# Kernel tuning notes

Hardware: AMD Instinct MI355X
Metric: run time of the kernel (lower is better)

Reference implementation:

```python
import jax, jax.numpy as jnp
import numpy as np

N_NODES = 80000
N_EDGES = 1280000
IN_DIM = 32
EDGE_DIM = 16
HID = 64
DEPTH = 4
BN_EPS = 1e-5
LN_EPS = 1e-5


def setup_inputs() -> dict:
    key = jax.random.key(0)
    ks = jax.random.split(key, 20)
    s = lambda fan: 1.0 / np.sqrt(fan)
    inp = {
        "x": jax.random.normal(ks[0], (N_NODES, IN_DIM), jnp.float32),
        "edge_index": jax.random.randint(ks[1], (2, N_EDGES), 0, N_NODES, jnp.int32),
        "edge_attr": jax.random.normal(ks[2], (N_EDGES, EDGE_DIM), jnp.float32),
        # input embeddings
        "Wx": jax.random.normal(ks[3], (IN_DIM, HID), jnp.float32) * s(IN_DIM),
        "bx": jnp.zeros((HID,), jnp.float32),
        "We": jax.random.normal(ks[4], (EDGE_DIM, HID), jnp.float32) * s(EDGE_DIM),
        "be": jnp.zeros((HID,), jnp.float32),
        # per-layer GIN MLP params (stacked over DEPTH)
        "W1": jax.random.normal(ks[5], (DEPTH, HID, 2 * HID), jnp.float32) * s(HID),
        "b1": jnp.zeros((DEPTH, 2 * HID), jnp.float32),
        "g1": jnp.ones((DEPTH, 2 * HID), jnp.float32),   # BatchNorm gamma
        "bt1": jnp.zeros((DEPTH, 2 * HID), jnp.float32),  # BatchNorm beta
        "W2": jax.random.normal(ks[6], (DEPTH, 2 * HID, HID), jnp.float32) * s(2 * HID),
        "b2": jnp.zeros((DEPTH, HID), jnp.float32),
        "eps": jnp.zeros((DEPTH,), jnp.float32),           # GIN epsilon, init 0
        # per-layer LayerNorm params
        "ln_g": jnp.ones((DEPTH, HID), jnp.float32),
        "ln_b": jnp.zeros((DEPTH, HID), jnp.float32),
    }
    return inp


def reference(x, edge_index, edge_attr, Wx, bx, We, be, W1, b1, g1, bt1, W2, b2, eps, ln_g, ln_b):
    n = x.shape[0]
    h = jax.nn.relu(x @ Wx + bx)                      # [N, HID]
    ea = jax.nn.relu(edge_attr @ We + be)             # [E, HID]
    row, col = edge_index[0], edge_index[1]           # source, target
    L = W1.shape[0]
    for l in range(L):
        # message: relu(x_j + edge_attr), scatter-add into target nodes
        msg = jax.nn.relu(h[row] + ea)                # [E, HID]
        agg = jax.ops.segment_sum(msg, col, num_segments=n)  # [N, HID]
        z = (1.0 + eps[l]) * h + agg
        # GIN MLP: Linear -> BatchNorm(train stats) -> ReLU -> Linear
        z = z @ W1[l] + b1[l]                         # [N, 2*HID]
        mu = z.mean(axis=0)
        var = z.var(axis=0)                           # biased, as torch BN training
        z = (z - mu) * jax.lax.rsqrt(var + BN_EPS) * g1[l] + bt1[l]
        z = jax.nn.relu(z)
        z = z @ W2[l] + b2[l]                         # [N, HID]
        # LayerNorm
        lm = z.mean(axis=-1, keepdims=True)
        lv = z.var(axis=-1, keepdims=True)
        z = (z - lm) * jax.lax.rsqrt(lv + LN_EPS) * ln_g[l] + ln_b[l]
        if l < L - 1:
            z = jax.nn.relu(z)
        h = z
    return h  # JK == 'last'
```

## Files before the change

kernel.cpp:

```cpp
#include <hip/hip_runtime.h>
#include <cstdint>

typedef _Float16 half8 __attribute__((ext_vector_type(8)));
typedef float f32x4 __attribute__((ext_vector_type(4)));

#define NNODES 80000
#define NEDGES 1280000
#define INDIM 32
#define EDIM 16
#define HID 64
#define HID2 128
#define DEPTH 4
#define BN_EPS 1e-5f
#define LN_EPS 1e-5f
#define NB 313

union U16x8 { uint4 v; _Float16 h[8]; };

__global__ __launch_bounds__(256) void k_node_embed(
    const float* __restrict__ x, const float* __restrict__ Wx,
    const float* __restrict__ bx, _Float16* __restrict__ h16) {
    int gw = (blockIdx.x * 256 + threadIdx.x) >> 6;
    int lane = threadIdx.x & 63;
    if (gw >= NNODES) return;
    float xv = (lane < INDIM) ? x[(size_t)gw * INDIM + lane] : 0.f;
    float acc = bx[lane];
#pragma unroll
    for (int k = 0; k < INDIM; k++)
        acc = fmaf(__shfl(xv, k, 64), Wx[k * HID + lane], acc);
    h16[(size_t)gw * HID + lane] = (_Float16)fmaxf(acc, 0.f);
}

__global__ __launch_bounds__(256) void k_prep(
    const float* __restrict__ W1, const float* __restrict__ W2,
    _Float16* __restrict__ w1T, _Float16* __restrict__ w2T) {
    int id = blockIdx.x * 256 + threadIdx.x;
    if (id < DEPTH * 128 * 64) {
        int l = id / 8192, r = id % 8192, n = r / 64, k = r % 64;
        w1T[id] = (_Float16)W1[(size_t)l * 8192 + k * 128 + n];
    } else {
        int idx = id - DEPTH * 128 * 64;
        int l = idx / 8192, r = idx % 8192, n = r / 128, k = r % 128;
        w2T[idx] = (_Float16)W2[(size_t)l * 8192 + k * 64 + n];
    }
}

__global__ __launch_bounds__(256) void k_hist(const int* __restrict__ col, int* __restrict__ deg) {
    int e = blockIdx.x * 256 + threadIdx.x;
    if (e < NEDGES) atomicAdd(&deg[col[e]], 1);
}

__global__ __launch_bounds__(256) void k_scan1(const int* __restrict__ deg, int* __restrict__ bsum) {
    __shared__ int s[256];
    int i = blockIdx.x * 256 + threadIdx.x;
    int v = (i < NNODES) ? deg[i] : 0;
    s[threadIdx.x] = v;
    __syncthreads();
    for (int o = 128; o > 0; o >>= 1) {
        if (threadIdx.x < o) s[threadIdx.x] += s[threadIdx.x + o];
        __syncthreads();
    }
    if (threadIdx.x == 0) bsum[blockIdx.x] = s[0];
}

__global__ __launch_bounds__(512) void k_scan2(const int* __restrict__ bsum, int* __restrict__ boff) {
    __shared__ int s[512];
    int t = threadIdx.x;
    s[t] = (t < NB) ? bsum[t] : 0;
    __syncthreads();
    for (int o = 1; o < 512; o <<= 1) {
        int v = (t >= o) ? s[t - o] : 0;
        __syncthreads();
        s[t] += v;
        __syncthreads();
    }
    if (t < NB) boff[t] = (t == 0) ? 0 : s[t - 1];
}

__global__ __launch_bounds__(256) void k_scan3(const int* __restrict__ deg,
                                               const int* __restrict__ boff,
                                               int* __restrict__ row_off) {
    __shared__ int s[256];
    int i = blockIdx.x * 256 + threadIdx.x;
    int t = threadIdx.x;
    int v = (i < NNODES) ? deg[i] : 0;
    s[t] = v;
    __syncthreads();
    for (int o = 1; o < 256; o <<= 1) {
        int u = (t >= o) ? s[t - o] : 0;
        __syncthreads();
        s[t] += u;
        __syncthreads();
    }
    int incl = s[t];
    if (i < NNODES) row_off[i] = boff[blockIdx.x] + incl - v;
    if (i == NNODES - 1) row_off[NNODES] = boff[blockIdx.x] + incl;
}

__global__ __launch_bounds__(256) void k_copy(const int* __restrict__ src, int* __restrict__ dst) {
    int i = blockIdx.x * 256 + threadIdx.x;
    if (i < NNODES) dst[i] = src[i];
}

__global__ __launch_bounds__(256) void k_scatter(const int* __restrict__ row,
                                                 const int* __restrict__ col,
                                                 int* __restrict__ cursor,
                                                 int* __restrict__ srow,
                                                 int* __restrict__ seid) {
    int e = blockIdx.x * 256 + threadIdx.x;
    if (e < NEDGES) {
        int c = col[e];
        int pos = atomicAdd(&cursor[c], 1);
        srow[pos] = row[e];
        seid[pos] = e;
    }
}

__global__ __launch_bounds__(256) void k_edge_embed(
    const float* __restrict__ eat, const int* __restrict__ seid,
    const float* __restrict__ We, const float* __restrict__ be,
    _Float16* __restrict__ eas) {
    __shared__ float wT[HID * EDIM];
    __shared__ float bs[HID];
    for (int i = threadIdx.x; i < HID * EDIM; i += 256) {
        int k = i & 15, o = i >> 4;
        wT[i] = We[k * HID + o];
    }
    if (threadIdx.x < HID) bs[threadIdx.x] = be[threadIdx.x];
    __syncthreads();
    int e = blockIdx.x * 256 + threadIdx.x;
    if (e >= NEDGES) return;
    int src = seid[e];
    const float4* ar = (const float4*)(eat + (size_t)src * EDIM);
    float4 a0 = ar[0], a1 = ar[1], a2 = ar[2], a3 = ar[3];
    float ev[16] = {a0.x, a0.y, a0.z, a0.w, a1.x, a1.y, a1.z, a1.w,
                    a2.x, a2.y, a2.z, a2.w, a3.x, a3.y, a3.z, a3.w};
    uint32_t outp[32];
#pragma unroll
    for (int o2 = 0; o2 < 32; o2++) {
        float acc[2];
#pragma unroll
        for (int half = 0; half < 2; half++) {
            int o = o2 * 2 + half;
            const float4* w4 = (const float4*)&wT[o * 16];
            float4 w0 = w4[0], w1 = w4[1], w2 = w4[2], w3 = w4[3];
            float p0 = fmaf(ev[3], w0.w, fmaf(ev[2], w0.z, fmaf(ev[1], w0.y, ev[0] * w0.x)));
            float p1 = fmaf(ev[7], w1.w, fmaf(ev[6], w1.z, fmaf(ev[5], w1.y, ev[4] * w1.x)));
            float p2 = fmaf(ev[11], w2.w, fmaf(ev[10], w2.z, fmaf(ev[9], w2.y, ev[8] * w2.x)));
            float p3 = fmaf(ev[15], w3.w, fmaf(ev[14], w3.z, fmaf(ev[13], w3.y, ev[12] * w3.x)));
            acc[half] = fmaxf(bs[o] + ((p0 + p1) + (p2 + p3)), 0.f);
        }
        union { _Float16 h[2]; uint32_t u; } pk;
        pk.h[0] = (_Float16)acc[0];
        pk.h[1] = (_Float16)acc[1];
        outp[o2] = pk.u;
    }
    uint4* dst = (uint4*)(eas + (size_t)e * HID);
#pragma unroll
    for (int q = 0; q < 8; q++)
        dst[q] = make_uint4(outp[q * 4], outp[q * 4 + 1], outp[q * 4 + 2], outp[q * 4 + 3]);
}

__global__ __launch_bounds__(256) void k_msg(
    const _Float16* __restrict__ h16, const int* __restrict__ row_off,
    const int* __restrict__ srow, const _Float16* __restrict__ eas,
    const float* __restrict__ epsp, _Float16* __restrict__ zc16) {
    int gw = (blockIdx.x * 256 + threadIdx.x) >> 6;
    int lane = threadIdx.x & 63;
    if (gw >= NNODES) return;
    int beg = row_off[gw], end = row_off[gw + 1];
    float acc = 0.f;
    int e = beg;
    for (; e + 7 < end; e += 8) {
        int j[8];
#pragma unroll
        for (int u = 0; u < 8; u++) j[u] = srow[e + u];
        float hv[8], ev[8];
#pragma unroll
        for (int u = 0; u < 8; u++) hv[u] = (float)h16[(size_t)j[u] * HID + lane];
#pragma unroll
        for (int u = 0; u < 8; u++) ev[u] = (float)eas[(size_t)(e + u) * HID + lane];
        float t0 = fmaxf(hv[0] + ev[0], 0.f) + fmaxf(hv[1] + ev[1], 0.f);
        float t1 = fmaxf(hv[2] + ev[2], 0.f) + fmaxf(hv[3] + ev[3], 0.f);
        float t2 = fmaxf(hv[4] + ev[4], 0.f) + fmaxf(hv[5] + ev[5], 0.f);
        float t3 = fmaxf(hv[6] + ev[6], 0.f) + fmaxf(hv[7] + ev[7], 0.f);
        acc += (t0 + t1) + (t2 + t3);
    }
    for (; e < end; ++e) {
        int j = srow[e];
        float hv = (float)h16[(size_t)j * HID + lane];
        float ev = (float)eas[(size_t)e * HID + lane];
        acc += fmaxf(hv + ev, 0.f);
    }
    float epsl = *epsp;
    float hv0 = (float)h16[(size_t)gw * HID + lane];
    zc16[(size_t)gw * HID + lane] = (_Float16)((1.f + epsl) * hv0 + acc);
}

__global__ __launch_bounds__(256) void k_gemm1(
    const _Float16* __restrict__ zc16, const _Float16* __restrict__ w1Tl,
    const float* __restrict__ b1l, _Float16* __restrict__ z1,
    float* __restrict__ bn_acc) {
    __shared__ __align__(16) unsigned char At[64 * 128];
    __shared__ __align__(16) unsigned char Bt[128 * 128];
    __shared__ float red[4][HID2][2];
    int tid = threadIdx.x;
    int nb = blockIdx.x * 64;
#pragma unroll
    for (int i = 0; i < 2; i++) {
        int id = tid + 256 * i;
        int node = id >> 3, c = id & 7;
        uint4 v = *(const uint4*)(zc16 + (size_t)(nb + node) * HID + c * 8);
        *(uint4*)(At + node * 128 + ((c ^ (node & 7)) << 4)) = v;
    }
#pragma unroll
    for (int i = 0; i < 4; i++) {
        int id = tid + 256 * i;
        int r = id >> 3, c = id & 7;
        uint4 v = *(const uint4*)(w1Tl + (size_t)r * HID + c * 8);
        *(uint4*)(Bt + r * 128 + ((c ^ (r & 7)) << 4)) = v;
    }
    __syncthreads();
    int lane = tid & 63, w = tid >> 6;
    int rl = lane & 15, b = lane >> 4;
    f32x4 acc[8];
#pragma unroll
    for (int t = 0; t < 8; t++) acc[t] = (f32x4){0.f, 0.f, 0.f, 0.f};
#pragma unroll
    for (int s = 0; s < 2; s++) {
        int arow = w * 16 + rl;
        half8 af = *(const half8*)(At + arow * 128 + (((s * 4 + b) ^ (rl & 7)) << 4));
#pragma unroll
        for (int t = 0; t < 8; t++) {
            int brow = t * 16 + rl;
            half8 bf = *(const half8*)(Bt + brow * 128 + (((s * 4 + b) ^ (rl & 7)) << 4));
            acc[t] = __builtin_amdgcn_mfma_f32_16x16x32_f16(af, bf, acc[t], 0, 0, 0);
        }
    }
#pragma unroll
    for (int t = 0; t < 8; t++) {
        int colg = t * 16 + rl;
        float bias = b1l[colg];
        float s = 0.f, q = 0.f;
#pragma unroll
        for (int r = 0; r < 4; r++) {
            float v = acc[t][r] + bias;
            int node = nb + w * 16 + b * 4 + r;
            z1[(size_t)node * HID2 + colg] = (_Float16)v;
            s += v;
            q = fmaf(v, v, q);
        }
        s += __shfl_xor(s, 16, 64); s += __shfl_xor(s, 32, 64);
        q += __shfl_xor(q, 16, 64); q += __shfl_xor(q, 32, 64);
        if (b == 0) { red[w][colg][0] = s; red[w][colg][1] = q; }
    }
    __syncthreads();
    int ch = tid & 127, which = tid >> 7;
    float tot = red[0][ch][which] + red[1][ch][which] + red[2][ch][which] + red[3][ch][which];
    atomicAdd(&bn_acc[which * HID2 + ch], tot);
}

__global__ void k_bnfin(const float* __restrict__ bn_acc,
                        const float* __restrict__ g1l,
                        const float* __restrict__ bt1l,
                        float* __restrict__ bn_sc) {
    int c = threadIdx.x;
    if (c >= HID2) return;
    float inv_n = 1.f / (float)NNODES;
    float mu = bn_acc[c] * inv_n;
    float ex2 = bn_acc[HID2 + c] * inv_n;
    float var = ex2 - mu * mu;
    float rs = rsqrtf(var + BN_EPS);
    float sc = g1l[c] * rs;
    bn_sc[c] = sc;
    bn_sc[HID2 + c] = bt1l[c] - mu * sc;
}

__global__ __launch_bounds__(256) void k_mlp2(
    const _Float16* __restrict__ z1, const float* __restrict__ bn_sc,
    const _Float16* __restrict__ w2Tl, const float* __restrict__ b2l,
    const float* __restrict__ lngl, const float* __restrict__ lnbl,
    int last, _Float16* __restrict__ hout, float* __restrict__ fout) {
    __shared__ __align__(16) unsigned char Yt[64 * 256];
    __shared__ __align__(16) unsigned char Wt[64 * 256];
    __shared__ float sbn[256];
    int tid = threadIdx.x;
    int nb = blockIdx.x * 64;
    sbn[tid] = bn_sc[tid];
#pragma unroll
    for (int i = 0; i < 4; i++) {
        int id = tid + 256 * i;
        int r = id >> 4, c = id & 15;
        uint4 v = *(const uint4*)(w2Tl + (size_t)r * HID2 + c * 8);
        *(uint4*)(Wt + r * 256 + ((c ^ (r & 7)) << 4)) = v;
    }
    __syncthreads();
#pragma unroll
    for (int i = 0; i < 4; i++) {
        int id = tid + 256 * i;
        int node = id >> 4, c = id & 15;
        U16x8 u, o;
        u.v = *(const uint4*)(z1 + (size_t)(nb + node) * HID2 + c * 8);
#pragma unroll
        for (int j = 0; j < 8; j++) {
            int chn = c * 8 + j;
            float y = fmaxf(fmaf((float)u.h[j], sbn[chn], sbn[HID2 + chn]), 0.f);
            o.h[j] = (_Float16)y;
        }
        *(uint4*)(Yt + node * 256 + ((c ^ (node & 7)) << 4)) = o.v;
    }
    __syncthreads();
    int lane = tid & 63, w = tid >> 6;
    int rl = lane & 15, b = lane >> 4;
    f32x4 acc[4];
#pragma unroll
    for (int t = 0; t < 4; t++) acc[t] = (f32x4){0.f, 0.f, 0.f, 0.f};
#pragma unroll
    for (int s = 0; s < 4; s++) {
        int arow = w * 16 + rl;
        half8 af = *(const half8*)(Yt + arow * 256 + (((s * 4 + b) ^ (rl & 7)) << 4));
#pragma unroll
        for (int t = 0; t < 4; t++) {
            int brow = t * 16 + rl;
            half8 bf = *(const half8*)(Wt + brow * 256 + (((s * 4 + b) ^ (rl & 7)) << 4));
            acc[t] = __builtin_amdgcn_mfma_f32_16x16x32_f16(af, bf, acc[t], 0, 0, 0);
        }
    }
    float a[4][4];
#pragma unroll
    for (int t = 0; t < 4; t++) {
        float bias = b2l[t * 16 + rl];
#pragma unroll
        for (int r = 0; r < 4; r++) a[r][t] = acc[t][r] + bias;
    }
    float m[4], vv[4];
#pragma unroll
    for (int r = 0; r < 4; r++) {
        float s = (a[r][0] + a[r][1]) + (a[r][2] + a[r][3]);
        s += __shfl_xor(s, 1, 64); s += __shfl_xor(s, 2, 64);
        s += __shfl_xor(s, 4, 64); s += __shfl_xor(s, 8, 64);
        m[r] = s * (1.f / 64.f);
    }
#pragma unroll
    for (int r = 0; r < 4; r++) {
        float t0 = a[r][0] - m[r], t1 = a[r][1] - m[r];
        float t2 = a[r][2] - m[r], t3 = a[r][3] - m[r];
        float q = (t0 * t0 + t1 * t1) + (t2 * t2 + t3 * t3);
        q += __shfl_xor(q, 1, 64); q += __shfl_xor(q, 2, 64);
        q += __shfl_xor(q, 4, 64); q += __shfl_xor(q, 8, 64);
        vv[r] = rsqrtf(q * (1.f / 64.f) + LN_EPS);
    }
#pragma unroll
    for (int t = 0; t < 4; t++) {
        int colg = t * 16 + rl;
        float lg = lngl[colg], lb = lnbl[colg];
#pragma unroll
        for (int r = 0; r < 4; r++) {
            float o = (a[r][t] - m[r]) * vv[r] * lg + lb;
            size_t node = nb + w * 16 + b * 4 + r;
            if (last) {
                fout[node * HID + colg] = o;
            } else {
                hout[node * HID + colg] = (_Float16)fmaxf(o, 0.f);
            }
        }
    }
}

extern "C" void kernel_launch(void* const* d_in, const int* in_sizes, int n_in,
                              void* d_out, int out_size, void* d_ws, size_t ws_size,
                              hipStream_t stream) {
    const float* x   = (const float*)d_in[0];
    const int*   ei  = (const int*)d_in[1];
    const float* eat = (const float*)d_in[2];
    const float* Wx  = (const float*)d_in[3];
    const float* bx  = (const float*)d_in[4];
    const float* We  = (const float*)d_in[5];
    const float* be  = (const float*)d_in[6];
    const float* W1  = (const float*)d_in[7];
    const float* b1  = (const float*)d_in[8];
    const float* g1  = (const float*)d_in[9];
    const float* bt1 = (const float*)d_in[10];
    const float* W2  = (const float*)d_in[11];
    const float* b2  = (const float*)d_in[12];
    const float* eps = (const float*)d_in[13];
    const float* lng = (const float*)d_in[14];
    const float* lnb = (const float*)d_in[15];
    const int* row = ei;
    const int* col = ei + NEDGES;

    char* p = (char*)d_ws;
    auto alloc = [&](size_t bytes) -> char* {
        char* r = p;
        p += (bytes + 255) & ~(size_t)255;
        return r;
    };
    _Float16* h16  = (_Float16*)alloc((size_t)NNODES * HID * 2);
    _Float16* zc16 = (_Float16*)alloc((size_t)NNODES * HID * 2);
    _Float16* z1   = (_Float16*)alloc((size_t)NNODES * HID2 * 2);
    int* row_off   = (int*)alloc((size_t)(NNODES + 1) * 4);
    int* srow      = (int*)alloc((size_t)NEDGES * 4);
    _Float16* eas  = (_Float16*)alloc((size_t)NEDGES * HID * 2);
    _Float16* w1T  = (_Float16*)alloc((size_t)DEPTH * 128 * 64 * 2);
    _Float16* w2T  = (_Float16*)alloc((size_t)DEPTH * 64 * 128 * 2);
    float* bn_acc  = (float*)alloc(256 * 4);
    float* bn_sc   = (float*)alloc(256 * 4);
    int* cursor = (int*)z1;
    int* seid   = (int*)z1 + NNODES;
    int* bsum   = (int*)z1 + NNODES + NEDGES;
    int* boff   = bsum + NB;
    (void)ws_size; (void)in_sizes; (void)n_in; (void)out_size;

    hipMemsetAsync(cursor, 0, (size_t)NNODES * 4, stream);
    k_node_embed<<<(NNODES + 3) / 4, 256, 0, stream>>>(x, Wx, bx, h16);
    k_prep<<<(DEPTH * 8192 * 2) / 256, 256, 0, stream>>>(W1, W2, w1T, w2T);
    k_hist<<<(NEDGES + 255) / 256, 256, 0, stream>>>(col, cursor);
    k_scan1<<<NB, 256, 0, stream>>>(cursor, bsum);
    k_scan2<<<1, 512, 0, stream>>>(bsum, boff);
    k_scan3<<<NB, 256, 0, stream>>>(cursor, boff, row_off);
    k_copy<<<NB, 256, 0, stream>>>(row_off, cursor);
    k_scatter<<<(NEDGES + 255) / 256, 256, 0, stream>>>(row, col, cursor, srow, seid);
    k_edge_embed<<<(NEDGES + 255) / 256, 256, 0, stream>>>(eat, seid, We, be, eas);

    const int msg_blocks = (NNODES + 3) / 4;
    const int mm_blocks = NNODES / 64;
    for (int l = 0; l < DEPTH; ++l) {
        k_msg<<<msg_blocks, 256, 0, stream>>>(h16, row_off, srow, eas, eps + l, zc16);
        hipMemsetAsync(bn_acc, 0, 256 * 4, stream);
        k_gemm1<<<mm_blocks, 256, 0, stream>>>(zc16, w1T + (size_t)l * 8192,
                                               b1 + (size_t)l * HID2, z1, bn_acc);
        k_bnfin<<<1, 128, 0, stream>>>(bn_acc, g1 + (size_t)l * HID2,
                                       bt1 + (size_t)l * HID2, bn_sc);
        k_mlp2<<<mm_blocks, 256, 0, stream>>>(z1, bn_sc, w2T + (size_t)l * 8192,
                                              b2 + (size_t)l * HID,
                                              lng + (size_t)l * HID, lnb + (size_t)l * HID,
                                              (l == DEPTH - 1) ? 1 : 0, h16, (float*)d_out);
    }
}
```

Before: 740.5 us.

## Compute edge embedding with MFMA and pack source/edge ids into one array

The edge embedding moves from per-thread scalar FMAs to 16x16x32 f16 MFMA instructions on a wavefront tile of 64 edges. Results are staged through a swizzled LDS buffer so each edge row is written out with coalesced stores. The scatter now writes (source, edge id) as one uint2 array instead of two int arrays, and k_msg reads the source index from it. That halves the density of the index reads in the per-layer message kernel, and the inputs are rounded to fp16 before the GEMM.

New measurement: 730.3 us. Within noise of the previous version (-1.4%).

```diff
diff --git a/kernel.cpp b/kernel.cpp
--- a/kernel.cpp
+++ b/kernel.cpp
@@ -105,65 +105,87 @@
 __global__ __launch_bounds__(256) void k_scatter(const int* __restrict__ row,
                                                  const int* __restrict__ col,
                                                  int* __restrict__ cursor,
-                                                 int* __restrict__ srow,
-                                                 int* __restrict__ seid) {
+                                                 uint2* __restrict__ sre) {
     int e = blockIdx.x * 256 + threadIdx.x;
     if (e < NEDGES) {
         int c = col[e];
         int pos = atomicAdd(&cursor[c], 1);
-        srow[pos] = row[e];
-        seid[pos] = e;
+        sre[pos] = make_uint2((unsigned)row[e], (unsigned)e);
     }
 }
 
 __global__ __launch_bounds__(256) void k_edge_embed(
-    const float* __restrict__ eat, const int* __restrict__ seid,
+    const float* __restrict__ eat, const uint2* __restrict__ sre,
     const float* __restrict__ We, const float* __restrict__ be,
     _Float16* __restrict__ eas) {
-    __shared__ float wT[HID * EDIM];
-    __shared__ float bs[HID];
-    for (int i = threadIdx.x; i < HID * EDIM; i += 256) {
-        int k = i & 15, o = i >> 4;
-        wT[i] = We[k * HID + o];
-    }
-    if (threadIdx.x < HID) bs[threadIdx.x] = be[threadIdx.x];
-    __syncthreads();
-    int e = blockIdx.x * 256 + threadIdx.x;
-    if (e >= NEDGES) return;
-    int src = seid[e];
-    const float4* ar = (const float4*)(eat + (size_t)src * EDIM);
+    __shared__ __align__(16) unsigned char lds[4][5120 + 8192];
+    int tid = threadIdx.x;
+    int w = tid >> 6, lane = tid & 63;
+    unsigned char* A = lds[w];
+    unsigned char* O = lds[w] + 5120;
+    int ebase = blockIdx.x * 256 + w * 64;
+    int b = lane >> 4, c = lane & 15;
+    half8 bf[4];
+#pragma unroll
+    for (int t = 0; t < 4; t++) {
+        half8 v = {};
+        if (b < 2) {
+#pragma unroll
+            for (int j = 0; j < 8; j++) {
+                int k = b * 8 + j;
+                v[j] = (_Float16)We[k * HID + t * 16 + c];
+            }
+        }
+        bf[t] = v;
+    }
+    float bias[4];
+#pragma unroll
+    for (int t = 0; t < 4; t++) bias[t] = be[t * 16 + c];
+    int eid = (int)sre[ebase + lane].y;
+    const float4* ar = (const float4*)(eat + (size_t)eid * EDIM);
     float4 a0 = ar[0], a1 = ar[1], a2 = ar[2], a3 = ar[3];
-    float ev[16] = {a0.x, a0.y, a0.z, a0.w, a1.x, a1.y, a1.z, a1.w,
-                    a2.x, a2.y, a2.z, a2.w, a3.x, a3.y, a3.z, a3.w};
-    uint32_t outp[32];
-#pragma unroll
-    for (int o2 = 0; o2 < 32; o2++) {
-        float acc[2];
-#pragma unroll
-        for (int half = 0; half < 2; half++) {
-            int o = o2 * 2 + half;
-            const float4* w4 = (const float4*)&wT[o * 16];
-            float4 w0 = w4[0], w1 = w4[1], w2 = w4[2], w3 = w4[3];
-            float p0 = fmaf(ev[3], w0.w, fmaf(ev[2], w0.z, fmaf(ev[1], w0.y, ev[0] * w0.x)));
-            float p1 = fmaf(ev[7], w1.w, fmaf(ev[6], w1.z, fmaf(ev[5], w1.y, ev[4] * w1.x)));
-            float p2 = fmaf(ev[11], w2.w, fmaf(ev[10], w2.z, fmaf(ev[9], w2.y, ev[8] * w2.x)));
-            float p3 = fmaf(ev[15], w3.w, fmaf(ev[14], w3.z, fmaf(ev[13], w3.y, ev[12] * w3.x)));
-            acc[half] = fmaxf(bs[o] + ((p0 + p1) + (p2 + p3)), 0.f);
-        }
-        union { _Float16 h[2]; uint32_t u; } pk;
-        pk.h[0] = (_Float16)acc[0];
-        pk.h[1] = (_Float16)acc[1];
-        outp[o2] = pk.u;
-    }
-    uint4* dst = (uint4*)(eas + (size_t)e * HID);
+    U16x8 lo, hi;
+    lo.h[0] = (_Float16)a0.x; lo.h[1] = (_Float16)a0.y;
+    lo.h[2] = (_Float16)a0.z; lo.h[3] = (_Float16)a0.w;
+    lo.h[4] = (_Float16)a1.x; lo.h[5] = (_Float16)a1.y;
+    lo.h[6] = (_Float16)a1.z; lo.h[7] = (_Float16)a1.w;
+    hi.h[0] = (_Float16)a2.x; hi.h[1] = (_Float16)a2.y;
+    hi.h[2] = (_Float16)a2.z; hi.h[3] = (_Float16)a2.w;
+    hi.h[4] = (_Float16)a3.x; hi.h[5] = (_Float16)a3.y;
+    hi.h[6] = (_Float16)a3.z; hi.h[7] = (_Float16)a3.w;
+    uint4 zz = make_uint4(0, 0, 0, 0);
+    *(uint4*)(A + lane * 80) = lo.v;
+    *(uint4*)(A + lane * 80 + 16) = hi.v;
+    *(uint4*)(A + lane * 80 + 32) = zz;
+    *(uint4*)(A + lane * 80 + 48) = zz;
+    __syncthreads();
+#pragma unroll
+    for (int it = 0; it < 4; it++) {
+        half8 af = *(const half8*)(A + (it * 16 + c) * 80 + b * 16);
+#pragma unroll
+        for (int t = 0; t < 4; t++) {
+            f32x4 acc = {0.f, 0.f, 0.f, 0.f};
+            acc = __builtin_amdgcn_mfma_f32_16x16x32_f16(af, bf[t], acc, 0, 0, 0);
+#pragma unroll
+            for (int r = 0; r < 4; r++) {
+                int erow = it * 16 + b * 4 + r;
+                int chan = t * 16 + c;
+                float v = fmaxf(acc[r] + bias[t], 0.f);
+                int byteoff = (erow * 128 + chan * 2) ^ ((erow & 7) << 4);
+                *(_Float16*)(O + byteoff) = (_Float16)v;
+            }
+        }
+    }
+    __syncthreads();
+    uint4* dst = (uint4*)(eas + (size_t)(ebase + lane) * HID);
 #pragma unroll
     for (int q = 0; q < 8; q++)
-        dst[q] = make_uint4(outp[q * 4], outp[q * 4 + 1], outp[q * 4 + 2], outp[q * 4 + 3]);
+        dst[q] = *(const uint4*)(O + ((lane * 128 + q * 16) ^ ((lane & 7) << 4)));
 }
 
 __global__ __launch_bounds__(256) void k_msg(
     const _Float16* __restrict__ h16, const int* __restrict__ row_off,
-    const int* __restrict__ srow, const _Float16* __restrict__ eas,
+    const uint2* __restrict__ sre, const _Float16* __restrict__ eas,
     const float* __restrict__ epsp, _Float16* __restrict__ zc16) {
     int gw = (blockIdx.x * 256 + threadIdx.x) >> 6;
     int lane = threadIdx.x & 63;
@@ -174,7 +196,7 @@
     for (; e + 7 < end; e += 8) {
         int j[8];
 #pragma unroll
-        for (int u = 0; u < 8; u++) j[u] = srow[e + u];
+        for (int u = 0; u < 8; u++) j[u] = (int)sre[e + u].x;
         float hv[8], ev[8];
 #pragma unroll
         for (int u = 0; u < 8; u++) hv[u] = (float)h16[(size_t)j[u] * HID + lane];
@@ -187,7 +209,7 @@
         acc += (t0 + t1) + (t2 + t3);
     }
     for (; e < end; ++e) {
-        int j = srow[e];
+        int j = (int)sre[e].x;
         float hv = (float)h16[(size_t)j * HID + lane];
         float ev = (float)eas[(size_t)e * HID + lane];
         acc += fmaxf(hv + ev, 0.f);
@@ -399,15 +421,14 @@
     _Float16* zc16 = (_Float16*)alloc((size_t)NNODES * HID * 2);
     _Float16* z1   = (_Float16*)alloc((size_t)NNODES * HID2 * 2);
     int* row_off   = (int*)alloc((size_t)(NNODES + 1) * 4);
-    int* srow      = (int*)alloc((size_t)NEDGES * 4);
+    uint2* sre     = (uint2*)alloc((size_t)NEDGES * 8);
     _Float16* eas  = (_Float16*)alloc((size_t)NEDGES * HID * 2);
     _Float16* w1T  = (_Float16*)alloc((size_t)DEPTH * 128 * 64 * 2);
     _Float16* w2T  = (_Float16*)alloc((size_t)DEPTH * 64 * 128 * 2);
     float* bn_acc  = (float*)alloc(256 * 4);
     float* bn_sc   = (float*)alloc(256 * 4);
     int* cursor = (int*)z1;
-    int* seid   = (int*)z1 + NNODES;
-    int* bsum   = (int*)z1 + NNODES + NEDGES;
+    int* bsum   = (int*)z1 + NNODES;
     int* boff   = bsum + NB;
     (void)ws_size; (void)in_sizes; (void)n_in; (void)out_size;
 
@@ -419,13 +440,13 @@
     k_scan2<<<1, 512, 0, stream>>>(bsum, boff);
     k_scan3<<<NB, 256, 0, stream>>>(cursor, boff, row_off);
     k_copy<<<NB, 256, 0, stream>>>(row_off, cursor);
-    k_scatter<<<(NEDGES + 255) / 256, 256, 0, stream>>>(row, col, cursor, srow, seid);
-    k_edge_embed<<<(NEDGES + 255) / 256, 256, 0, stream>>>(eat, seid, We, be, eas);
+    k_scatter<<<(NEDGES + 255) / 256, 256, 0, stream>>>(row, col, cursor, sre);
+    k_edge_embed<<<NEDGES / 256, 256, 0, stream>>>(eat, sre, We, be, eas);
 
     const int msg_blocks = (NNODES + 3) / 4;
     const int mm_blocks = NNODES / 64;
     for (int l = 0; l < DEPTH; ++l) {
-        k_msg<<<msg_blocks, 256, 0, stream>>>(h16, row_off, srow, eas, eps + l, zc16);
+        k_msg<<<msg_blocks, 256, 0, stream>>>(h16, row_off, sre, eas, eps + l, zc16);
         hipMemsetAsync(bn_acc, 0, 256 * 4, stream);
         k_gemm1<<<mm_blocks, 256, 0, stream>>>(zc16, w1T + (size_t)l * 8192,
                                                b1 + (size_t)l * HID2, z1, bn_acc);
```
